# Kernel optimization log

Measured on AMD Instinct MI355X. Metric: run time of the kernel, lower is better.

## Reference

```python
import jax, jax.numpy as jnp
import numpy as np

INPUT_SIZE = 1024
MODULE_SIZE = 256   # k
N_MODULES = 8       # g
HIDDEN = MODULE_SIZE * N_MODULES
T = 4096
PERIODS = jnp.array([2 ** i for i in range(N_MODULES)], dtype=jnp.int32)  # [1,2,...,128]


def setup_inputs() -> dict:
    key = jax.random.key(0)
    k1, k2, k3, k4, k5 = jax.random.split(key, 5)
    s = 1.0 / np.sqrt(HIDDEN)
    return {
        "x": jax.random.normal(k1, (T, INPUT_SIZE), dtype=jnp.float32),
        "W_ih": jax.random.normal(k2, (HIDDEN, INPUT_SIZE), dtype=jnp.float32) * s,
        "W_hh": jax.random.normal(k3, (HIDDEN, HIDDEN), dtype=jnp.float32) * s,
        "b_ih": jax.random.normal(k4, (HIDDEN,), dtype=jnp.float32) * s,
        "b_hh": jax.random.normal(k5, (HIDDEN,), dtype=jnp.float32) * s,
    }


def reference(x, W_ih, W_hh, b_ih, b_hh):
    # Clockwork RNN: at step t (1-indexed, curr_t starts at 1 for hx=None),
    # module j is active iff t % period_j == 0. Masking the weight columns
    # (rows of W^T) is equivalent to masking the pre-activation output, and
    # tanh(0)=0 so inactive modules keep their previous hidden value.
    ts = jnp.arange(1, x.shape[0] + 1, dtype=jnp.int32)

    def step(h, inp):
        xt, t = inp  # xt: (input_size,), t: scalar int
        mask = jnp.repeat((t % PERIODS) == 0, MODULE_SIZE).astype(h.dtype)  # (H,)
        pre = xt @ W_ih.T + b_ih + h @ W_hh.T + b_hh                        # (H,)
        h_new = h * (1.0 - mask) + jnp.tanh(pre * mask)
        return h_new, h_new

    h0 = jnp.zeros((HIDDEN,), dtype=x.dtype)
    _, outs = jax.lax.scan(step, h0, (x, ts))
    return outs  # (T, HIDDEN)
```

## Files before the change

### kernel.cpp

```cpp
#include <hip/hip_runtime.h>
#include <math.h>

#define T_STEPS 4096
#define HID     2048
#define MOD     256
#define INSZ    1024
#define NWAVE   256

static __device__ __forceinline__ unsigned long long agent_load_u64(
        const unsigned long long* p) {
    return __hip_atomic_load((unsigned long long*)p, __ATOMIC_RELAXED,
                             __HIP_MEMORY_SCOPE_AGENT);
}
static __device__ __forceinline__ void agent_store_u64(
        unsigned long long* p, unsigned long long v) {
    __hip_atomic_store(p, v, __ATOMIC_RELAXED, __HIP_MEMORY_SCOPE_AGENT);
}

#define BM 128
#define BN 128
#define BK 8

__global__ __launch_bounds__(256) void gemm_u(
    const float* __restrict__ x, const float* __restrict__ Wih,
    const float* __restrict__ bih, const float* __restrict__ bhh,
    float* __restrict__ out)
{
    __shared__ float As[BK][BM];
    __shared__ float Bs[BK][BN];

    const int tid = threadIdx.x;
    const int t0 = blockIdx.y * BM;
    const int i0 = blockIdx.x * BN;
    const int tx = tid & 15;
    const int ty = tid >> 4;
    const int arow = tid >> 1;
    const int acol = (tid & 1) * 4;

    float acc[8][8];
#pragma unroll
    for (int a = 0; a < 8; ++a)
#pragma unroll
        for (int b = 0; b < 8; ++b) acc[a][b] = 0.0f;

    for (int k0 = 0; k0 < INSZ; k0 += BK) {
        float4 av = *(const float4*)(x   + (size_t)(t0 + arow) * INSZ + k0 + acol);
        float4 bv = *(const float4*)(Wih + (size_t)(i0 + arow) * INSZ + k0 + acol);
        __syncthreads();
        As[acol + 0][arow] = av.x; As[acol + 1][arow] = av.y;
        As[acol + 2][arow] = av.z; As[acol + 3][arow] = av.w;
        Bs[acol + 0][arow] = bv.x; Bs[acol + 1][arow] = bv.y;
        Bs[acol + 2][arow] = bv.z; Bs[acol + 3][arow] = bv.w;
        __syncthreads();
#pragma unroll
        for (int kk = 0; kk < BK; ++kk) {
            float a[8], b[8];
            *(float4*)&a[0] = *(const float4*)&As[kk][ty * 8];
            *(float4*)&a[4] = *(const float4*)&As[kk][ty * 8 + 4];
            *(float4*)&b[0] = *(const float4*)&Bs[kk][tx * 8];
            *(float4*)&b[4] = *(const float4*)&Bs[kk][tx * 8 + 4];
#pragma unroll
            for (int ri = 0; ri < 8; ++ri)
#pragma unroll
                for (int ci = 0; ci < 8; ++ci)
                    acc[ri][ci] = fmaf(a[ri], b[ci], acc[ri][ci]);
        }
    }

    float bias[8];
#pragma unroll
    for (int ci = 0; ci < 8; ++ci) {
        int i = i0 + tx * 8 + ci;
        bias[ci] = bih[i] + bhh[i];
    }
#pragma unroll
    for (int ri = 0; ri < 8; ++ri) {
        int t = t0 + ty * 8 + ri;
#pragma unroll
        for (int ci = 0; ci < 8; ++ci) {
            int i = i0 + tx * 8 + ci;
            out[(size_t)t * HID + i] = acc[ri][ci] + bias[ci];
        }
    }
}

__global__ __launch_bounds__(64, 1) void cwrnn_rec(
    float* __restrict__ out, const float* __restrict__ Whh,
    unsigned long long* __restrict__ comm)
{
    const int lane = threadIdx.x;
    const int g    = blockIdx.x;

    float4 hreg[8];
#pragma unroll
    for (int j = 0; j < 8; ++j) hreg[j] = make_float4(0.f, 0.f, 0.f, 0.f);

    float4 w0[8];
    {
        const float4* wr = (const float4*)(Whh + (size_t)g * HID);
#pragma unroll
        for (int j = 0; j < 8; ++j) w0[j] = wr[lane + 64 * j];
    }

    for (int t = 1; t <= T_STEPS; ++t) {
        const int ctz = __builtin_ctz(t);
        const int A = (ctz + 1 > 8) ? 8 : (ctz + 1);
        float* orow = out + (size_t)(t - 1) * HID;

        float upf = (lane < A) ? orow[lane * MOD + g] : 0.0f;

        if (t > 1) {
            const int ctzp = __builtin_ctz(t - 1);
            const int Ap = (ctzp + 1 > 8) ? 8 : (ctzp + 1);
            const unsigned need = (unsigned)(t - 1);
            const unsigned long long* csrc =
                comm + (size_t)((t - 1) & 1) * HID + 4 * lane;
            unsigned long long pv[8][4];
            for (;;) {
#pragma unroll
                for (int j = 0; j < 8; ++j) {
                    if (j < Ap) {
                        pv[j][0] = agent_load_u64(csrc + j * MOD + 0);
                        pv[j][1] = agent_load_u64(csrc + j * MOD + 1);
                        pv[j][2] = agent_load_u64(csrc + j * MOD + 2);
                        pv[j][3] = agent_load_u64(csrc + j * MOD + 3);
                    }
                }
                bool ok = true;
#pragma unroll
                for (int j = 0; j < 8; ++j) {
                    if (j < Ap)
                        ok = ok && ((unsigned)(pv[j][0] >> 32) >= need)
                                && ((unsigned)(pv[j][1] >> 32) >= need)
                                && ((unsigned)(pv[j][2] >> 32) >= need)
                                && ((unsigned)(pv[j][3] >> 32) >= need);
                }
                if (ok) break;
            }
#pragma unroll
            for (int j = 0; j < 8; ++j) {
                if (j < Ap)
                    hreg[j] = make_float4(
                        __uint_as_float((unsigned)pv[j][0]),
                        __uint_as_float((unsigned)pv[j][1]),
                        __uint_as_float((unsigned)pv[j][2]),
                        __uint_as_float((unsigned)pv[j][3]));
            }
        }

        unsigned long long* cdst = comm + (size_t)(t & 1) * HID;
        const unsigned long long tagbits =
            ((unsigned long long)(unsigned)t) << 32;

        {
            float4 s = make_float4(0.f, 0.f, 0.f, 0.f);
#pragma unroll
            for (int j = 0; j < 8; ++j) {
                s.x = fmaf(w0[j].x, hreg[j].x, s.x);
                s.y = fmaf(w0[j].y, hreg[j].y, s.y);
                s.z = fmaf(w0[j].z, hreg[j].z, s.z);
                s.w = fmaf(w0[j].w, hreg[j].w, s.w);
            }
            float acc = (s.x + s.y) + (s.z + s.w);
#pragma unroll
            for (int off = 32; off; off >>= 1) acc += __shfl_xor(acc, off, 64);
            float u0 = __shfl(upf, 0, 64);
            if (lane == 0) {
                float hv = tanhf(u0 + acc);
                agent_store_u64(cdst + g,
                    tagbits | (unsigned long long)__float_as_uint(hv));
                orow[g] = hv;
            }
        }

        int m = 1;
        for (; m + 1 < A; m += 2) {
            const int ra = m * MOD + g;
            const int rb = ra + MOD;
            const float4* wa = (const float4*)(Whh + (size_t)ra * HID);
            const float4* wb = (const float4*)(Whh + (size_t)rb * HID);
            float4 sa = make_float4(0.f, 0.f, 0.f, 0.f);
            float4 sb = make_float4(0.f, 0.f, 0.f, 0.f);
#pragma unroll
            for (int j = 0; j < 8; ++j) {
                float4 a = wa[lane + 64 * j];
                float4 b = wb[lane + 64 * j];
                sa.x = fmaf(a.x, hreg[j].x, sa.x);
                sa.y = fmaf(a.y, hreg[j].y, sa.y);
                sa.z = fmaf(a.z, hreg[j].z, sa.z);
                sa.w = fmaf(a.w, hreg[j].w, sa.w);
                sb.x = fmaf(b.x, hreg[j].x, sb.x);
                sb.y = fmaf(b.y, hreg[j].y, sb.y);
                sb.z = fmaf(b.z, hreg[j].z, sb.z);
                sb.w = fmaf(b.w, hreg[j].w, sb.w);
            }
            float acca = (sa.x + sa.y) + (sa.z + sa.w);
            float accb = (sb.x + sb.y) + (sb.z + sb.w);
#pragma unroll
            for (int off = 32; off; off >>= 1) {
                acca += __shfl_xor(acca, off, 64);
                accb += __shfl_xor(accb, off, 64);
            }
            float ua = __shfl(upf, m, 64);
            float ub = __shfl(upf, m + 1, 64);
            if (lane == 0) {
                float hva = tanhf(ua + acca);
                float hvb = tanhf(ub + accb);
                agent_store_u64(cdst + ra,
                    tagbits | (unsigned long long)__float_as_uint(hva));
                agent_store_u64(cdst + rb,
                    tagbits | (unsigned long long)__float_as_uint(hvb));
                orow[ra] = hva;
                orow[rb] = hvb;
            }
        }
        if (m < A) {
            const int r = m * MOD + g;
            const float4* wr = (const float4*)(Whh + (size_t)r * HID);
            float4 s = make_float4(0.f, 0.f, 0.f, 0.f);
#pragma unroll
            for (int j = 0; j < 8; ++j) {
                float4 a = wr[lane + 64 * j];
                s.x = fmaf(a.x, hreg[j].x, s.x);
                s.y = fmaf(a.y, hreg[j].y, s.y);
                s.z = fmaf(a.z, hreg[j].z, s.z);
                s.w = fmaf(a.w, hreg[j].w, s.w);
            }
            float acc = (s.x + s.y) + (s.z + s.w);
#pragma unroll
            for (int off = 32; off; off >>= 1) acc += __shfl_xor(acc, off, 64);
            float um = __shfl(upf, m, 64);
            if (lane == 0) {
                float hv = tanhf(um + acc);
                agent_store_u64(cdst + r,
                    tagbits | (unsigned long long)__float_as_uint(hv));
                orow[r] = hv;
            }
        }

#pragma unroll
        for (int j = 0; j < 8; ++j) {
            if (j >= A && g == (j - A)) {
                *(float4*)(orow + j * MOD + 4 * lane) = hreg[j];
            }
        }
    }
}

extern "C" void kernel_launch(void* const* d_in, const int* in_sizes, int n_in,
                              void* d_out, int out_size, void* d_ws, size_t ws_size,
                              hipStream_t stream) {
    const float* x   = (const float*)d_in[0];
    const float* Wih = (const float*)d_in[1];
    const float* Whh = (const float*)d_in[2];
    const float* bih = (const float*)d_in[3];
    const float* bhh = (const float*)d_in[4];
    float* out = (float*)d_out;
    unsigned long long* comm = (unsigned long long*)d_ws;

    hipMemsetAsync(d_ws, 0, 2 * HID * sizeof(unsigned long long), stream);

    dim3 g1(HID / BN, T_STEPS / BM);
    gemm_u<<<g1, 256, 0, stream>>>(x, Wih, bih, bhh, out);
    cwrnn_rec<<<NWAVE, 64, 0, stream>>>(out, Whh, comm);
}
```

Before: 11.20 ms.

## Replicate tagged hidden-state exchange buffers across 16 reader groups

Each producer wave now writes its tagged hidden values into 16 replicated communication buffers, one per group of 16 consumer waves. Each consumer polls only its group's copy. The aim is to spread polling traffic across more cache lines and memory channels, so fewer waves spin on the same lines and cross-workgroup synchronization gets cheaper. In exchange, every step issues 16x more stores, and the workspace and memset grow 16x.

```diff
diff --git a/kernel.cpp b/kernel.cpp
--- a/kernel.cpp
+++ b/kernel.cpp
@@ -6,6 +6,7 @@
 #define MOD     256
 #define INSZ    1024
 #define NWAVE   256
+#define NREP    16
 
 static __device__ __forceinline__ unsigned long long agent_load_u64(
         const unsigned long long* p) {
@@ -90,6 +91,7 @@
 {
     const int lane = threadIdx.x;
     const int g    = blockIdx.x;
+    const int grp  = g >> 4;
 
     float4 hreg[8];
 #pragma unroll
@@ -114,7 +116,7 @@
             const int Ap = (ctzp + 1 > 8) ? 8 : (ctzp + 1);
             const unsigned need = (unsigned)(t - 1);
             const unsigned long long* csrc =
-                comm + (size_t)((t - 1) & 1) * HID + 4 * lane;
+                comm + (size_t)(grp * 2 + ((t - 1) & 1)) * HID + 4 * lane;
             unsigned long long pv[8][4];
             for (;;) {
 #pragma unroll
@@ -148,7 +150,7 @@
             }
         }
 
-        unsigned long long* cdst = comm + (size_t)(t & 1) * HID;
+        const size_t pbase = (size_t)(t & 1) * HID;
         const unsigned long long tagbits =
             ((unsigned long long)(unsigned)t) << 32;
 
@@ -165,12 +167,12 @@
 #pragma unroll
             for (int off = 32; off; off >>= 1) acc += __shfl_xor(acc, off, 64);
             float u0 = __shfl(upf, 0, 64);
-            if (lane == 0) {
-                float hv = tanhf(u0 + acc);
-                agent_store_u64(cdst + g,
-                    tagbits | (unsigned long long)__float_as_uint(hv));
-                orow[g] = hv;
-            }
+            float hv = tanhf(u0 + acc);
+            unsigned long long pkt =
+                tagbits | (unsigned long long)__float_as_uint(hv);
+            if (lane < NREP)
+                agent_store_u64(comm + (size_t)(lane * 2) * HID + pbase + g, pkt);
+            if (lane == 0) orow[g] = hv;
         }
 
         int m = 1;
@@ -203,16 +205,18 @@
             }
             float ua = __shfl(upf, m, 64);
             float ub = __shfl(upf, m + 1, 64);
-            if (lane == 0) {
-                float hva = tanhf(ua + acca);
-                float hvb = tanhf(ub + accb);
-                agent_store_u64(cdst + ra,
-                    tagbits | (unsigned long long)__float_as_uint(hva));
-                agent_store_u64(cdst + rb,
-                    tagbits | (unsigned long long)__float_as_uint(hvb));
-                orow[ra] = hva;
-                orow[rb] = hvb;
-            }
+            float hva = tanhf(ua + acca);
+            float hvb = tanhf(ub + accb);
+            unsigned long long pa =
+                tagbits | (unsigned long long)__float_as_uint(hva);
+            unsigned long long pb =
+                tagbits | (unsigned long long)__float_as_uint(hvb);
+            if (lane < NREP) {
+                unsigned long long* rb_ = comm + (size_t)(lane * 2) * HID + pbase;
+                agent_store_u64(rb_ + ra, pa);
+                agent_store_u64(rb_ + rb, pb);
+            }
+            if (lane == 0) { orow[ra] = hva; orow[rb] = hvb; }
         }
         if (m < A) {
             const int r = m * MOD + g;
@@ -230,12 +234,12 @@
 #pragma unroll
             for (int off = 32; off; off >>= 1) acc += __shfl_xor(acc, off, 64);
             float um = __shfl(upf, m, 64);
-            if (lane == 0) {
-                float hv = tanhf(um + acc);
-                agent_store_u64(cdst + r,
-                    tagbits | (unsigned long long)__float_as_uint(hv));
-                orow[r] = hv;
-            }
+            float hv = tanhf(um + acc);
+            unsigned long long pkt =
+                tagbits | (unsigned long long)__float_as_uint(hv);
+            if (lane < NREP)
+                agent_store_u64(comm + (size_t)(lane * 2) * HID + pbase + r, pkt);
+            if (lane == 0) orow[r] = hv;
         }
 
 #pragma unroll
@@ -258,7 +262,8 @@
     float* out = (float*)d_out;
     unsigned long long* comm = (unsigned long long*)d_ws;
 
-    hipMemsetAsync(d_ws, 0, 2 * HID * sizeof(unsigned long long), stream);
+    hipMemsetAsync(d_ws, 0, (size_t)NREP * 2 * HID * sizeof(unsigned long long),
+                   stream);
 
     dim3 g1(HID / BN, T_STEPS / BM);
     gemm_u<<<g1, 256, 0, stream>>>(x, Wih, bih, bhh, out);
```

Result: slower. 16.21 ms (+44.8%).

## Split recurrence into fast module-0 blocks with delta updates and even-step slow workers

Applied to the files above, without the earlier changes.

The recurrent kernel is restructured. Eight dedicated blocks compute the period-1 module every step, holding their W_hh rows in registers and updating the dot product incrementally from deltas of changed hidden values staged in shared memory. Separate workgroups handle the slower modules only on even steps. The slower modules publish through their own double-buffered tagged channel and also write their outputs ahead into the next row. This aims to shorten the per-step critical path for the module that updates every step, and tanhf is replaced by an exp-based fast tanh. The cost is that the incremental delta accumulation can drift numerically, and the spin-waits now have bail-out counters that could silently give up.

```diff
diff --git a/kernel.cpp b/kernel.cpp
--- a/kernel.cpp
+++ b/kernel.cpp
@@ -5,16 +5,30 @@
 #define HID     2048
 #define MOD     256
 #define INSZ    1024
-#define NWAVE   256
-
-static __device__ __forceinline__ unsigned long long agent_load_u64(
-        const unsigned long long* p) {
-    return __hip_atomic_load((unsigned long long*)p, __ATOMIC_RELAXED,
-                             __HIP_MEMORY_SCOPE_AGENT);
-}
-static __device__ __forceinline__ void agent_store_u64(
-        unsigned long long* p, unsigned long long v) {
+#define REST    1792
+#define NFAST   8
+#define NWIDEB  32
+
+typedef unsigned long long u64;
+
+static __device__ __forceinline__ u64 agent_load_u64(const u64* p) {
+    return __hip_atomic_load((u64*)p, __ATOMIC_RELAXED, __HIP_MEMORY_SCOPE_AGENT);
+}
+static __device__ __forceinline__ void agent_store_u64(u64* p, u64 v) {
     __hip_atomic_store(p, v, __ATOMIC_RELAXED, __HIP_MEMORY_SCOPE_AGENT);
+}
+static __device__ __forceinline__ u64 mkpkt(int t, float v) {
+    return ((u64)(unsigned)t << 32) | (u64)__float_as_uint(v);
+}
+static __device__ __forceinline__ unsigned ptag(u64 v) { return (unsigned)(v >> 32); }
+static __device__ __forceinline__ float    pval(u64 v) { return __uint_as_float((unsigned)v); }
+static __device__ __forceinline__ int nact(int t) {
+    int a = __builtin_ctz(t) + 1; return a > 8 ? 8 : a;
+}
+static __device__ __forceinline__ float tanh_fast(float x) {
+    x = fminf(fmaxf(x, -15.f), 15.f);
+    float e = __expf(2.f * x);
+    return (e - 1.f) / (e + 1.f);
 }
 
 #define BM 128
@@ -84,164 +98,210 @@
     }
 }
 
-__global__ __launch_bounds__(64, 1) void cwrnn_rec(
+__global__ __launch_bounds__(512) void cwrnn_rec(
     float* __restrict__ out, const float* __restrict__ Whh,
-    unsigned long long* __restrict__ comm)
+    u64* __restrict__ comm)
 {
-    const int lane = threadIdx.x;
-    const int g    = blockIdx.x;
-
-    float4 hreg[8];
-#pragma unroll
-    for (int j = 0; j < 8; ++j) hreg[j] = make_float4(0.f, 0.f, 0.f, 0.f);
-
-    float4 w0[8];
-    {
-        const float4* wr = (const float4*)(Whh + (size_t)g * HID);
-#pragma unroll
-        for (int j = 0; j < 8; ++j) w0[j] = wr[lane + 64 * j];
-    }
-
-    for (int t = 1; t <= T_STEPS; ++t) {
-        const int ctz = __builtin_ctz(t);
-        const int A = (ctz + 1 > 8) ? 8 : (ctz + 1);
-        float* orow = out + (size_t)(t - 1) * HID;
-
-        float upf = (lane < A) ? orow[lane * MOD + g] : 0.0f;
-
-        if (t > 1) {
-            const int ctzp = __builtin_ctz(t - 1);
-            const int Ap = (ctzp + 1 > 8) ? 8 : (ctzp + 1);
-            const unsigned need = (unsigned)(t - 1);
-            const unsigned long long* csrc =
-                comm + (size_t)((t - 1) & 1) * HID + 4 * lane;
-            unsigned long long pv[8][4];
-            for (;;) {
+    u64* h0c = comm;
+    u64* rc  = comm + 512;
+
+    __shared__ float dlt[HID];
+
+    if (blockIdx.x < NFAST) {
+        const int tau = threadIdx.x;
+        const int r   = (blockIdx.x << 5) + (tau >> 4);
+        const int lam = tau & 15;
+
+        float wreg[128];
+        {
+            const float* wr = Whh + (size_t)r * HID + lam;
+#pragma unroll
+            for (int k = 0; k < 128; ++k) wreg[k] = wr[16 * k];
+        }
+        float D = 0.f;
+        float old0 = 0.f;
+        float oldr0 = 0.f, oldr1 = 0.f, oldr2 = 0.f, oldr3 = 0.f;
+
+        for (int t = 1; t <= T_STEPS; ++t) {
+            float Upf = out[(size_t)(t - 1) * HID + r];
+
+            if (t > 1) {
+                const int Ap = nact(t - 1);
+                const unsigned need = (unsigned)(t - 1);
+
+                if (tau < 256) {
+                    const u64* p = h0c + (size_t)((t - 1) & 1) * MOD + tau;
+                    u64 v = agent_load_u64(p);
+                    int bail = 1 << 27;
+                    while (ptag(v) < need && --bail) v = agent_load_u64(p);
+                    float nv = pval(v);
+                    dlt[tau] = nv - old0; old0 = nv;
+                }
+                if ((t & 1) && Ap >= 2 && tau < 64 * (Ap - 1)) {
+                    const u64* p = rc + (size_t)(((t - 1) >> 1) & 1) * REST + 4 * tau;
+                    u64 v0 = agent_load_u64(p + 0), v1 = agent_load_u64(p + 1);
+                    u64 v2 = agent_load_u64(p + 2), v3 = agent_load_u64(p + 3);
+                    int bail = 1 << 27;
+                    while ((ptag(v0) < need || ptag(v1) < need ||
+                            ptag(v2) < need || ptag(v3) < need) && --bail) {
+                        v0 = agent_load_u64(p + 0); v1 = agent_load_u64(p + 1);
+                        v2 = agent_load_u64(p + 2); v3 = agent_load_u64(p + 3);
+                    }
+                    const int c = 256 + 4 * tau;
+                    float n0 = pval(v0), n1 = pval(v1), n2 = pval(v2), n3 = pval(v3);
+                    dlt[c + 0] = n0 - oldr0; oldr0 = n0;
+                    dlt[c + 1] = n1 - oldr1; oldr1 = n1;
+                    dlt[c + 2] = n2 - oldr2; oldr2 = n2;
+                    dlt[c + 3] = n3 - oldr3; oldr3 = n3;
+                }
+                __syncthreads();
+
+                float acc = 0.f;
+#pragma unroll
+                for (int mm = 0; mm < 8; ++mm) {
+                    if (mm < Ap) {
+#pragma unroll
+                        for (int kk = 0; kk < 16; ++kk)
+                            acc = fmaf(wreg[mm * 16 + kk],
+                                       dlt[mm * MOD + lam + 16 * kk], acc);
+                    }
+                }
+                acc += __shfl_xor(acc, 1, 64);
+                acc += __shfl_xor(acc, 2, 64);
+                acc += __shfl_xor(acc, 4, 64);
+                acc += __shfl_xor(acc, 8, 64);
+                D += acc;
+            }
+
+            float hv = tanh_fast(Upf + D);
+            if (lam == 0) {
+                agent_store_u64(h0c + (size_t)(t & 1) * MOD + r, mkpkt(t, hv));
+                out[(size_t)(t - 1) * HID + r] = hv;
+            }
+            __syncthreads();
+        }
+    } else {
+        const int lane = threadIdx.x & 63;
+        const int w    = (blockIdx.x - NFAST) * 8 + (threadIdx.x >> 6);
+
+        float4 hreg[8];
+#pragma unroll
+        for (int j = 0; j < 8; ++j) hreg[j] = make_float4(0.f, 0.f, 0.f, 0.f);
+
+        for (int t = 2; t <= T_STEPS; t += 2) {
+            const int A = nact(t);
+            float* orow = out + (size_t)(t - 1) * HID;
+            float upf = (lane >= 1 && lane < A) ? orow[lane * MOD + w] : 0.f;
+
+            if (t >= 4) {
+                const int Ar = nact(t - 2);
+                const unsigned needr = (unsigned)(t - 2);
+                const u64* rp = rc + (size_t)(((t - 2) >> 1) & 1) * REST + 4 * lane;
+#pragma unroll
+                for (int m = 1; m < 8; ++m) {
+                    if (m < Ar) {
+                        const u64* p = rp + (m - 1) * MOD;
+                        u64 v0 = agent_load_u64(p + 0), v1 = agent_load_u64(p + 1);
+                        u64 v2 = agent_load_u64(p + 2), v3 = agent_load_u64(p + 3);
+                        int bail = 1 << 27;
+                        while ((ptag(v0) < needr || ptag(v1) < needr ||
+                                ptag(v2) < needr || ptag(v3) < needr) && --bail) {
+                            v0 = agent_load_u64(p + 0); v1 = agent_load_u64(p + 1);
+                            v2 = agent_load_u64(p + 2); v3 = agent_load_u64(p + 3);
+                        }
+                        hreg[m] = make_float4(pval(v0), pval(v1), pval(v2), pval(v3));
+                    }
+                }
+            }
+            {
+                const unsigned need = (unsigned)(t - 1);
+                const u64* p = h0c + MOD + 4 * lane;
+                u64 v0 = agent_load_u64(p + 0), v1 = agent_load_u64(p + 1);
+                u64 v2 = agent_load_u64(p + 2), v3 = agent_load_u64(p + 3);
+                int bail = 1 << 27;
+                while ((ptag(v0) < need || ptag(v1) < need ||
+                        ptag(v2) < need || ptag(v3) < need) && --bail) {
+                    __builtin_amdgcn_s_sleep(1);
+                    v0 = agent_load_u64(p + 0); v1 = agent_load_u64(p + 1);
+                    v2 = agent_load_u64(p + 2); v3 = agent_load_u64(p + 3);
+                }
+                hreg[0] = make_float4(pval(v0), pval(v1), pval(v2), pval(v3));
+            }
+
+#pragma unroll
+            for (int j = 1; j < 8; ++j) {
+                if (j >= A && w == (j - A)) {
+                    *(float4*)(orow + j * MOD + 4 * lane) = hreg[j];
+                    if (t < T_STEPS)
+                        *(float4*)(orow + HID + j * MOD + 4 * lane) = hreg[j];
+                }
+            }
+            if (t == 2 && w < 7)
+                *(float4*)(out + (size_t)(w + 1) * MOD + 4 * lane) =
+                    make_float4(0.f, 0.f, 0.f, 0.f);
+
+            u64* rdst = rc + (size_t)((t >> 1) & 1) * REST;
+            int m = 1;
+            for (; m + 1 < A; m += 2) {
+                const int ra = m * MOD + w;
+                const int rb2 = ra + MOD;
+                const float4* wa = (const float4*)(Whh + (size_t)ra * HID);
+                const float4* wb = (const float4*)(Whh + (size_t)rb2 * HID);
+                float4 sa = make_float4(0.f, 0.f, 0.f, 0.f);
+                float4 sb = make_float4(0.f, 0.f, 0.f, 0.f);
 #pragma unroll
                 for (int j = 0; j < 8; ++j) {
-                    if (j < Ap) {
-                        pv[j][0] = agent_load_u64(csrc + j * MOD + 0);
-                        pv[j][1] = agent_load_u64(csrc + j * MOD + 1);
-                        pv[j][2] = agent_load_u64(csrc + j * MOD + 2);
-                        pv[j][3] = agent_load_u64(csrc + j * MOD + 3);
-                    }
-                }
-                bool ok = true;
+                    float4 a = wa[lane + 64 * j];
+                    float4 b = wb[lane + 64 * j];
+                    sa.x = fmaf(a.x, hreg[j].x, sa.x);
+                    sa.y = fmaf(a.y, hreg[j].y, sa.y);
+                    sa.z = fmaf(a.z, hreg[j].z, sa.z);
+                    sa.w = fmaf(a.w, hreg[j].w, sa.w);
+                    sb.x = fmaf(b.x, hreg[j].x, sb.x);
+                    sb.y = fmaf(b.y, hreg[j].y, sb.y);
+                    sb.z = fmaf(b.z, hreg[j].z, sb.z);
+                    sb.w = fmaf(b.w, hreg[j].w, sb.w);
+                }
+                float acca = (sa.x + sa.y) + (sa.z + sa.w);
+                float accb = (sb.x + sb.y) + (sb.z + sb.w);
+#pragma unroll
+                for (int off = 32; off; off >>= 1) {
+                    acca += __shfl_xor(acca, off, 64);
+                    accb += __shfl_xor(accb, off, 64);
+                }
+                float ua = __shfl(upf, m, 64);
+                float ub = __shfl(upf, m + 1, 64);
+                float hva = tanh_fast(ua + acca);
+                float hvb = tanh_fast(ub + accb);
+                if (lane == 0) {
+                    agent_store_u64(rdst + (ra - MOD),  mkpkt(t, hva));
+                    agent_store_u64(rdst + (rb2 - MOD), mkpkt(t, hvb));
+                    orow[ra] = hva; orow[rb2] = hvb;
+                    if (t < T_STEPS) { orow[HID + ra] = hva; orow[HID + rb2] = hvb; }
+                }
+            }
+            if (m < A) {
+                const int rr = m * MOD + w;
+                const float4* wr = (const float4*)(Whh + (size_t)rr * HID);
+                float4 s = make_float4(0.f, 0.f, 0.f, 0.f);
 #pragma unroll
                 for (int j = 0; j < 8; ++j) {
-                    if (j < Ap)
-                        ok = ok && ((unsigned)(pv[j][0] >> 32) >= need)
-                                && ((unsigned)(pv[j][1] >> 32) >= need)
-                                && ((unsigned)(pv[j][2] >> 32) >= need)
-                                && ((unsigned)(pv[j][3] >> 32) >= need);
-                }
-                if (ok) break;
-            }
-#pragma unroll
-            for (int j = 0; j < 8; ++j) {
-                if (j < Ap)
-                    hreg[j] = make_float4(
-                        __uint_as_float((unsigned)pv[j][0]),
-                        __uint_as_float((unsigned)pv[j][1]),
-                        __uint_as_float((unsigned)pv[j][2]),
-                        __uint_as_float((unsigned)pv[j][3]));
-            }
-        }
-
-        unsigned long long* cdst = comm + (size_t)(t & 1) * HID;
-        const unsigned long long tagbits =
-            ((unsigned long long)(unsigned)t) << 32;
-
-        {
-            float4 s = make_float4(0.f, 0.f, 0.f, 0.f);
-#pragma unroll
-            for (int j = 0; j < 8; ++j) {
-                s.x = fmaf(w0[j].x, hreg[j].x, s.x);
-                s.y = fmaf(w0[j].y, hreg[j].y, s.y);
-                s.z = fmaf(w0[j].z, hreg[j].z, s.z);
-                s.w = fmaf(w0[j].w, hreg[j].w, s.w);
-            }
-            float acc = (s.x + s.y) + (s.z + s.w);
-#pragma unroll
-            for (int off = 32; off; off >>= 1) acc += __shfl_xor(acc, off, 64);
-            float u0 = __shfl(upf, 0, 64);
-            if (lane == 0) {
-                float hv = tanhf(u0 + acc);
-                agent_store_u64(cdst + g,
-                    tagbits | (unsigned long long)__float_as_uint(hv));
-                orow[g] = hv;
-            }
-        }
-
-        int m = 1;
-        for (; m + 1 < A; m += 2) {
-            const int ra = m * MOD + g;
-            const int rb = ra + MOD;
-            const float4* wa = (const float4*)(Whh + (size_t)ra * HID);
-            const float4* wb = (const float4*)(Whh + (size_t)rb * HID);
-            float4 sa = make_float4(0.f, 0.f, 0.f, 0.f);
-            float4 sb = make_float4(0.f, 0.f, 0.f, 0.f);
-#pragma unroll
-            for (int j = 0; j < 8; ++j) {
-                float4 a = wa[lane + 64 * j];
-                float4 b = wb[lane + 64 * j];
-                sa.x = fmaf(a.x, hreg[j].x, sa.x);
-                sa.y = fmaf(a.y, hreg[j].y, sa.y);
-                sa.z = fmaf(a.z, hreg[j].z, sa.z);
-                sa.w = fmaf(a.w, hreg[j].w, sa.w);
-                sb.x = fmaf(b.x, hreg[j].x, sb.x);
-                sb.y = fmaf(b.y, hreg[j].y, sb.y);
-                sb.z = fmaf(b.z, hreg[j].z, sb.z);
-                sb.w = fmaf(b.w, hreg[j].w, sb.w);
-            }
-            float acca = (sa.x + sa.y) + (sa.z + sa.w);
-            float accb = (sb.x + sb.y) + (sb.z + sb.w);
-#pragma unroll
-            for (int off = 32; off; off >>= 1) {
-                acca += __shfl_xor(acca, off, 64);
-                accb += __shfl_xor(accb, off, 64);
-            }
-            float ua = __shfl(upf, m, 64);
-            float ub = __shfl(upf, m + 1, 64);
-            if (lane == 0) {
-                float hva = tanhf(ua + acca);
-                float hvb = tanhf(ub + accb);
-                agent_store_u64(cdst + ra,
-                    tagbits | (unsigned long long)__float_as_uint(hva));
-                agent_store_u64(cdst + rb,
-                    tagbits | (unsigned long long)__float_as_uint(hvb));
-                orow[ra] = hva;
-                orow[rb] = hvb;
-            }
-        }
-        if (m < A) {
-            const int r = m * MOD + g;
-            const float4* wr = (const float4*)(Whh + (size_t)r * HID);
-            float4 s = make_float4(0.f, 0.f, 0.f, 0.f);
-#pragma unroll
-            for (int j = 0; j < 8; ++j) {
-                float4 a = wr[lane + 64 * j];
-                s.x = fmaf(a.x, hreg[j].x, s.x);
-                s.y = fmaf(a.y, hreg[j].y, s.y);
-                s.z = fmaf(a.z, hreg[j].z, s.z);
-                s.w = fmaf(a.w, hreg[j].w, s.w);
-            }
-            float acc = (s.x + s.y) + (s.z + s.w);
-#pragma unroll
-            for (int off = 32; off; off >>= 1) acc += __shfl_xor(acc, off, 64);
-            float um = __shfl(upf, m, 64);
-            if (lane == 0) {
-                float hv = tanhf(um + acc);
-                agent_store_u64(cdst + r,
-                    tagbits | (unsigned long long)__float_as_uint(hv));
-                orow[r] = hv;
-            }
-        }
-
-#pragma unroll
-        for (int j = 0; j < 8; ++j) {
-            if (j >= A && g == (j - A)) {
-                *(float4*)(orow + j * MOD + 4 * lane) = hreg[j];
+                    float4 a = wr[lane + 64 * j];
+                    s.x = fmaf(a.x, hreg[j].x, s.x);
+                    s.y = fmaf(a.y, hreg[j].y, s.y);
+                    s.z = fmaf(a.z, hreg[j].z, s.z);
+                    s.w = fmaf(a.w, hreg[j].w, s.w);
+                }
+                float acc = (s.x + s.y) + (s.z + s.w);
+#pragma unroll
+                for (int off = 32; off; off >>= 1) acc += __shfl_xor(acc, off, 64);
+                float um = __shfl(upf, m, 64);
+                float hv = tanh_fast(um + acc);
+                if (lane == 0) {
+                    agent_store_u64(rdst + (rr - MOD), mkpkt(t, hv));
+                    orow[rr] = hv;
+                    if (t < T_STEPS) orow[HID + rr] = hv;
+                }
             }
         }
     }
@@ -256,11 +316,11 @@
     const float* bih = (const float*)d_in[3];
     const float* bhh = (const float*)d_in[4];
     float* out = (float*)d_out;
-    unsigned long long* comm = (unsigned long long*)d_ws;
-
-    hipMemsetAsync(d_ws, 0, 2 * HID * sizeof(unsigned long long), stream);
+    u64* comm = (u64*)d_ws;
+
+    hipMemsetAsync(d_ws, 0, (size_t)(512 + 2 * REST) * sizeof(u64), stream);
 
     dim3 g1(HID / BN, T_STEPS / BM);
     gemm_u<<<g1, 256, 0, stream>>>(x, Wih, bih, bhh, out);
-    cwrnn_rec<<<NWAVE, 64, 0, stream>>>(out, Whh, comm);
-}
+    cwrnn_rec<<<NFAST + NWIDEB, 512, 0, stream>>>(out, Whh, comm);
+}
```

Result: slower. 18.83 ms (+68.1%).
